# Performance work log

Hardware: AMD Instinct MI355X
Metric: run time of the kernel (lower is better)

The kernel has to match this reference:

```python
import jax, jax.numpy as jnp
import numpy as np

K = 7        # kernal_size
STRIDE = 1
PAD = 3      # padding (reflect)
M = K // 2   # center tap index
GAMA = 0.5
EPS = 1e-09


def interp_linear(x, n_out):
    # torch F.interpolate(mode='linear', align_corners=False) on last dim. x: (b, c, n_in)
    n_in = x.shape[-1]
    src = (jnp.arange(n_out, dtype=jnp.float32) + 0.5) * (n_in / n_out) - 0.5
    src = jnp.clip(src, 0.0, n_in - 1.0)
    lo = jnp.floor(src).astype(jnp.int32)
    hi = jnp.minimum(lo + 1, n_in - 1)
    w = (src - lo.astype(jnp.float32)).astype(x.dtype)
    return x[..., lo] * (1.0 - w) + x[..., hi] * w


def unfold1d(x, k, s, p):
    # x: (b, c, n) -> windows (b, L, c, k), matching F.unfold's c-major/k-minor layout
    if p > 0:
        x = jnp.pad(x, ((0, 0), (0, 0), (p, p)), mode='reflect')
    n = x.shape[-1]
    L = (n - k) // s + 1
    idx = jnp.arange(L)[:, None] * s + jnp.arange(k)[None, :]  # (L, k)
    win = x[:, :, idx]                                          # (b, c, L, k)
    return jnp.transpose(win, (0, 2, 1, 3))                     # (b, L, c, k)


def setup_inputs() -> dict:
    key = jax.random.key(0)
    k1, k2, k3, k4, k5 = jax.random.split(key, 5)
    b, dc, nd = 16, 16, 1024
    c_in, c_out, n = 64, 128, 4096
    deep = jax.random.normal(k1, (b, dc, nd), dtype=jnp.float32)
    x = jax.random.normal(k2, (b, c_in, n), dtype=jnp.float32)
    conv_w = jax.random.normal(k3, (c_in, dc), dtype=jnp.float32) * (1.0 / np.sqrt(dc))
    conv_b = jax.random.normal(k4, (c_in,), dtype=jnp.float32) * 0.02
    fc_w = jax.random.normal(k5, (c_out, c_in * K), dtype=jnp.float32) * (1.0 / np.sqrt(c_in * K))
    return {"deep": deep, "x": x, "conv_w": conv_w, "conv_b": conv_b, "fc_w": fc_w}


def reference(deep, x, conv_w, conv_b, fc_w):
    b, c, n = x.shape
    # --- get_deep_loss ---
    xr = interp_linear(deep, n)                                  # (b, dc, n)
    y = jnp.einsum('bdn,cd->bcn', xr, conv_w) + conv_b[None, :, None]
    mean = jnp.mean(y, axis=2, keepdims=True)
    var = jnp.var(y, axis=2, keepdims=True, ddof=1)              # torch var_mean unbiased
    xs = GAMA * (y - mean) / (var + EPS)                         # DeepShuffle1d
    x1 = unfold1d(xs, K, STRIDE, PAD)                            # (b, L, c, k)
    d = jnp.abs(x1 - x1[..., M:M + 1])
    loss = 1.0 - jnp.tanh(d) ** 2                                # (b, L, c, k)
    alpha = 1.0 / jnp.sum(loss, axis=-1, keepdims=True)          # (b, L, c, 1)
    deep_loss = (loss * alpha).reshape(b, -1, c * K)             # (b, L, c*k)
    # --- deep_conv ---
    y1 = unfold1d(x, K, STRIDE, PAD).reshape(b, -1, c * K)       # (b, L, c*k)
    out = jnp.einsum('blf,of->bol', deep_loss * y1, fc_w)        # (b, c_out, L)
    return out
```

## Files before the change

kernel.cpp:

```cpp
#include <hip/hip_runtime.h>
#include <hip/hip_bf16.h>
#include <math.h>

namespace {
typedef __attribute__((ext_vector_type(8)))  short  short8;
typedef __attribute__((ext_vector_type(4)))  float  floatx4;
typedef _Float16 f16;
typedef __attribute__((ext_vector_type(4)))  _Float16 half4;

constexpr int Bc = 16;
constexpr int DC = 16;
constexpr int ND = 1024;
constexpr int C  = 64;
constexpr int N  = 4096;
constexpr int CO = 128;
constexpr int KW = 7;
constexpr int F  = C * KW;
constexpr int LT = 32;
constexpr int PLD = F + 8;

__device__ inline unsigned short f2bf(float f) {
    __hip_bfloat16 h = __float2bfloat16(f);
    return __builtin_bit_cast(unsigned short, h);
}

__global__ __launch_bounds__(256)
void k1(const float* __restrict__ deep, const float* __restrict__ conv_w,
        const float* __restrict__ conv_b, const float* __restrict__ fcw,
        f16* __restrict__ xs, unsigned short* __restrict__ wb)
{
    if (blockIdx.x >= Bc * C) {
        const int i = ((blockIdx.x - Bc * C) * 256 + threadIdx.x) * 4;
        const float4 v = *(const float4*)(fcw + i);
        ushort4 o;
        o.x = f2bf(v.x); o.y = f2bf(v.y); o.z = f2bf(v.z); o.w = f2bf(v.w);
        *(ushort4*)(wb + i) = o;
        return;
    }
    const int b = blockIdx.x >> 6;
    const int c = blockIdx.x & 63;
    const int tid = threadIdx.x;
    __shared__ float V[ND];
    __shared__ float r1[256], r2[256];

    float cw[DC];
#pragma unroll
    for (int d = 0; d < DC; ++d) cw[d] = conv_w[c * DC + d];
    const float cb = conv_b[c];
    const float* dp = deep + b * DC * ND;

#pragma unroll
    for (int p = 0; p < 4; ++p) {
        const int t = tid + 256 * p;
        float a = 0.f;
#pragma unroll
        for (int d = 0; d < DC; ++d) a = fmaf(dp[d * ND + t], cw[d], a);
        V[t] = a;
    }
    __syncthreads();

    float s1 = 0.f, s2 = 0.f;
#pragma unroll
    for (int it = 0; it < 4; ++it) {
        const int g = tid + 256 * it;
        const float vm = V[g == 0 ? 0 : g - 1];
        const float v0 = V[g];
        const float vp = V[g == ND - 1 ? ND - 1 : g + 1];
        const float y0 = fmaf(0.375f, vm, fmaf(0.625f, v0, cb));
        const float y1 = fmaf(0.125f, vm, fmaf(0.875f, v0, cb));
        const float y2 = fmaf(0.125f, vp, fmaf(0.875f, v0, cb));
        const float y3 = fmaf(0.375f, vp, fmaf(0.625f, v0, cb));
        s1 += (y0 + y1) + (y2 + y3);
        s2 = fmaf(y0, y0, s2); s2 = fmaf(y1, y1, s2);
        s2 = fmaf(y2, y2, s2); s2 = fmaf(y3, y3, s2);
    }
    r1[tid] = s1; r2[tid] = s2;
    __syncthreads();
    for (int off = 128; off > 0; off >>= 1) {
        if (tid < off) { r1[tid] += r1[tid + off]; r2[tid] += r2[tid + off]; }
        __syncthreads();
    }
    const float mean = r1[0] * (1.f / N);
    const float var  = (r2[0] - (float)N * mean * mean) * (1.f / (N - 1));
    const float sc   = 0.5f / (var + 1e-9f);

    f16* xsp = xs + (b * C + c) * N;
#pragma unroll
    for (int it = 0; it < 4; ++it) {
        const int g = tid + 256 * it;
        const float vm = V[g == 0 ? 0 : g - 1];
        const float v0 = V[g];
        const float vp = V[g == ND - 1 ? ND - 1 : g + 1];
        half4 h;
        h.x = (f16)((fmaf(0.375f, vm, fmaf(0.625f, v0, cb)) - mean) * sc);
        h.y = (f16)((fmaf(0.125f, vm, fmaf(0.875f, v0, cb)) - mean) * sc);
        h.z = (f16)((fmaf(0.125f, vp, fmaf(0.875f, v0, cb)) - mean) * sc);
        h.w = (f16)((fmaf(0.375f, vp, fmaf(0.625f, v0, cb)) - mean) * sc);
        *(half4*)(xsp + 4 * g) = h;
    }
}

__global__ __launch_bounds__(256)
void k2(const f16* __restrict__ xs, const float* __restrict__ x,
        const unsigned short* __restrict__ wb, float* __restrict__ out)
{
    __shared__ __align__(16) unsigned short phi[LT * PLD];
    const int b   = blockIdx.y;
    const int l0  = blockIdx.x * LT;
    const int tid = threadIdx.x;

#pragma unroll
    for (int p = 0; p < (LT * C) / 256; ++p) {
        const int id = tid + 256 * p;
        const int l = id & (LT - 1);
        const int c = id >> 5;
        const int gl = l0 + l;
        const f16*  xsp = xs + (b * C + c) * N;
        const float* xp = x  + (b * C + c) * N;
        const float center = (float)xsp[gl];
        float lossv[KW], xv[KW];
        float lsum = 0.f;
#pragma unroll
        for (int k = 0; k < KW; ++k) {
            int q = gl + k - 3;
            q = (q < 0) ? -q : ((q >= N) ? (2 * N - 2 - q) : q);
            const float v = (float)xsp[q];
            xv[k] = xp[q];
            const float d = fabsf(v - center);
            const float e = __expf(-2.f * d);
            const float t = 1.f + e;
            const float lo = 4.f * e / (t * t);
            lossv[k] = lo;
            lsum += lo;
        }
        const float alpha = 1.f / lsum;
        unsigned short* pr = phi + l * PLD + c * KW;
#pragma unroll
        for (int k = 0; k < KW; ++k) pr[k] = f2bf(lossv[k] * alpha * xv[k]);
    }
    __syncthreads();

    const int wv   = tid >> 6;
    const int lane = tid & 63;
    const int quad = lane >> 4;
    const int rr   = lane & 15;
    const int o0   = wv * 32;

    floatx4 acc00 = {0.f, 0.f, 0.f, 0.f}, acc01 = acc00, acc10 = acc00, acc11 = acc00;
    const unsigned short* wrow0 = wb + (o0 + rr) * F + quad * 8;
    const unsigned short* wrow1 = wrow0 + 16 * F;
    const unsigned short* prow0 = phi + rr * PLD + quad * 8;
    const unsigned short* prow1 = prow0 + 16 * PLD;

    for (int s = 0; s < F / 32; ++s) {
        const int f0 = 32 * s;
        const short8 a0 = *(const short8*)(wrow0 + f0);
        const short8 a1 = *(const short8*)(wrow1 + f0);
        const short8 b0 = *(const short8*)(prow0 + f0);
        const short8 b1 = *(const short8*)(prow1 + f0);
        acc00 = __builtin_amdgcn_mfma_f32_16x16x32_bf16(a0, b0, acc00, 0, 0, 0);
        acc01 = __builtin_amdgcn_mfma_f32_16x16x32_bf16(a0, b1, acc01, 0, 0, 0);
        acc10 = __builtin_amdgcn_mfma_f32_16x16x32_bf16(a1, b0, acc10, 0, 0, 0);
        acc11 = __builtin_amdgcn_mfma_f32_16x16x32_bf16(a1, b1, acc11, 0, 0, 0);
    }

    float* ob = out + (b * CO) * N + l0;
#pragma unroll
    for (int i = 0; i < 4; ++i) {
        const int om = quad * 4 + i;
        ob[(o0 + om) * N      + rr     ] = acc00[i];
        ob[(o0 + om) * N      + 16 + rr] = acc01[i];
        ob[(o0 + 16 + om) * N + rr     ] = acc10[i];
        ob[(o0 + 16 + om) * N + 16 + rr] = acc11[i];
    }
}
}

extern "C" void kernel_launch(void* const* d_in, const int* in_sizes, int n_in,
                              void* d_out, int out_size, void* d_ws, size_t ws_size,
                              hipStream_t stream)
{
    const float* deep   = (const float*)d_in[0];
    const float* x      = (const float*)d_in[1];
    const float* conv_w = (const float*)d_in[2];
    const float* conv_b = (const float*)d_in[3];
    const float* fc_w   = (const float*)d_in[4];
    float* out = (float*)d_out;

    f16* xs = (f16*)d_ws;
    unsigned short* wb = (unsigned short*)((char*)d_ws + (8u << 20));

    hipLaunchKernelGGL(k1, dim3(Bc * C + 56), dim3(256), 0, stream,
                       deep, conv_w, conv_b, fc_w, xs, wb);
    hipLaunchKernelGGL(k2, dim3(N / LT, Bc), dim3(256), 0, stream,
                       xs, x, wb, out);
}
```

Baseline: 123.8 us.

## Vectorize phi construction with per-thread 8-position windows and fast reciprocals

The prologue of k2 is remapped so each thread owns one channel and eight consecutive positions. It loads a 14-element halo once with vector half8/float4 loads instead of issuing seven scalar gathers per output. The centre tap is fixed at 0.25 rather than recomputed, and the divisions are replaced by hardware reciprocal approximations. This cuts redundant global loads and ALU work, but the phi stores become strided across threads (channel-major), which may cause LDS bank conflicts. The fast reciprocals also slightly reduce precision.

```diff
diff --git a/kernel.cpp b/kernel.cpp
--- a/kernel.cpp
+++ b/kernel.cpp
@@ -7,6 +7,7 @@
 typedef __attribute__((ext_vector_type(4)))  float  floatx4;
 typedef _Float16 f16;
 typedef __attribute__((ext_vector_type(4)))  _Float16 half4;
+typedef __attribute__((ext_vector_type(8)))  _Float16 half8;
 
 constexpr int Bc = 16;
 constexpr int DC = 16;
@@ -23,6 +24,7 @@
     __hip_bfloat16 h = __float2bfloat16(f);
     return __builtin_bit_cast(unsigned short, h);
 }
+__device__ inline float rcpf(float x) { return __builtin_amdgcn_rcpf(x); }
 
 __global__ __launch_bounds__(256)
 void k1(const float* __restrict__ deep, const float* __restrict__ conv_w,
@@ -109,34 +111,65 @@
     const int l0  = blockIdx.x * LT;
     const int tid = threadIdx.x;
 
-#pragma unroll
-    for (int p = 0; p < (LT * C) / 256; ++p) {
-        const int id = tid + 256 * p;
-        const int l = id & (LT - 1);
-        const int c = id >> 5;
-        const int gl = l0 + l;
-        const f16*  xsp = xs + (b * C + c) * N;
-        const float* xp = x  + (b * C + c) * N;
-        const float center = (float)xsp[gl];
-        float lossv[KW], xv[KW];
-        float lsum = 0.f;
-#pragma unroll
-        for (int k = 0; k < KW; ++k) {
-            int q = gl + k - 3;
-            q = (q < 0) ? -q : ((q >= N) ? (2 * N - 2 - q) : q);
-            const float v = (float)xsp[q];
-            xv[k] = xp[q];
-            const float d = fabsf(v - center);
-            const float e = __expf(-2.f * d);
-            const float t = 1.f + e;
-            const float lo = 4.f * e / (t * t);
-            lossv[k] = lo;
-            lsum += lo;
+    {
+        const int c    = tid & 63;
+        const int seg  = tid >> 6;
+        const int base = l0 + seg * 8;
+        const f16*   xsr = xs + (b * C + c) * N;
+        const float* xr  = x  + (b * C + c) * N;
+
+        float vs[14], xv[14];
+        const bool edge = (blockIdx.x == 0 && seg == 0) ||
+                          (blockIdx.x == (N / LT - 1) && seg == 3);
+        if (!edge) {
+            const half8 a0 = *(const half8*)(xsr + base - 8);
+            const half8 a1 = *(const half8*)(xsr + base);
+            const half8 a2 = *(const half8*)(xsr + base + 8);
+            const float4 x0 = *(const float4*)(xr + base - 4);
+            const float4 x1 = *(const float4*)(xr + base);
+            const float4 x2 = *(const float4*)(xr + base + 4);
+            const float4 x3 = *(const float4*)(xr + base + 8);
+            const float xf[16] = {x0.x, x0.y, x0.z, x0.w, x1.x, x1.y, x1.z, x1.w,
+                                  x2.x, x2.y, x2.z, x2.w, x3.x, x3.y, x3.z, x3.w};
+#pragma unroll
+            for (int i = 0; i < 14; ++i) {
+                const int j = 5 + i;
+                const f16 v = (j < 8) ? a0[j] : ((j < 16) ? a1[j - 8] : a2[j - 16]);
+                vs[i] = (float)v;
+                xv[i] = xf[1 + i];
+            }
+        } else {
+#pragma unroll
+            for (int i = 0; i < 14; ++i) {
+                int p = base - 3 + i;
+                p = (p < 0) ? -p : ((p >= N) ? (2 * N - 2 - p) : p);
+                vs[i] = (float)xsr[p];
+                xv[i] = xr[p];
+            }
         }
-        const float alpha = 1.f / lsum;
-        unsigned short* pr = phi + l * PLD + c * KW;
-#pragma unroll
-        for (int k = 0; k < KW; ++k) pr[k] = f2bf(lossv[k] * alpha * xv[k]);
+
+        unsigned short* pcol = phi + c * KW;
+#pragma unroll
+        for (int li = 0; li < 8; ++li) {
+            const float cen = vs[li + 3];
+            float u[KW];
+            float s = 0.25f;
+            u[3] = 0.25f;
+#pragma unroll
+            for (int k = 0; k < KW; ++k) {
+                if (k == 3) continue;
+                const float d = fabsf(vs[li + k] - cen);
+                const float e = __expf(-2.f * d);
+                const float t = 1.f + e;
+                const float uk = e * rcpf(t * t);
+                u[k] = uk;
+                s += uk;
+            }
+            const float al = rcpf(s);
+            unsigned short* pr = pcol + (seg * 8 + li) * PLD;
+#pragma unroll
+            for (int k = 0; k < KW; ++k) pr[k] = f2bf(u[k] * al * xv[li + k]);
+        }
     }
     __syncthreads();
 
```

Result: no change. 125.2 us (+1.1%).
